# Kernel tuning notes

Measured on AMD Instinct MI355X. Metric: run time of the kernel, lower is better.

The kernel has to match this reference:

```python
import jax, jax.numpy as jnp
import numpy as np


def setup_inputs() -> dict:
    key = jax.random.key(0)
    ks = jax.random.split(key, 10)
    B, S, H, I, V = 64, 2048, 512, 512, 50257
    scale = 0.05
    return {
        "last_output": jax.random.randint(ks[0], (B,), 0, V),
        "last_hidden": jax.random.normal(ks[1], (1, B, H), jnp.float32),
        "encoder_outputs": jax.random.normal(ks[2], (S, B, H), jnp.float32),
        "embedding": jax.random.normal(ks[3], (V, I), jnp.float32) * scale,
        "W_ih": jax.random.normal(ks[4], (3 * H, I + H), jnp.float32) * scale,
        "b_ih": jax.random.normal(ks[5], (3 * H,), jnp.float32) * scale,
        "W_hh": jax.random.normal(ks[6], (3 * H, H), jnp.float32) * scale,
        "b_hh": jax.random.normal(ks[7], (3 * H,), jnp.float32) * scale,
        "W_out": jax.random.normal(ks[8], (V, 2 * H), jnp.float32) * scale,
        "b_out": jax.random.normal(ks[9], (V,), jnp.float32) * scale,
    }


def _gru_step(x, h, W_ih, b_ih, W_hh, b_hh):
    # torch nn.GRU parametrization, single layer, single timestep.
    H = h.shape[-1]
    gi = x @ W_ih.T + b_ih  # [B, 3H]
    gh = h @ W_hh.T + b_hh  # [B, 3H]
    i_r, i_z, i_n = gi[:, :H], gi[:, H:2 * H], gi[:, 2 * H:]
    h_r, h_z, h_n = gh[:, :H], gh[:, H:2 * H], gh[:, 2 * H:]
    r = jax.nn.sigmoid(i_r + h_r)
    z = jax.nn.sigmoid(i_z + h_z)
    n = jnp.tanh(i_n + r * h_n)
    return (1.0 - z) * n + z * h


def reference(last_output, last_hidden, encoder_outputs, embedding,
              W_ih, b_ih, W_hh, b_hh, W_out, b_out):
    # Embedding lookup: [B, I]
    embedded = embedding[last_output]
    h_top = last_hidden[-1]  # [B, H]
    # Luong 'dot' attention: score(b, s) = h_b . enc[s, b]
    scores = jnp.einsum('bh,sbh->bs', h_top, encoder_outputs)  # [B, S]
    attn = jax.nn.softmax(scores, axis=-1)                      # [B, S]
    # context = attn @ enc (per batch): [B, H]
    context = jnp.einsum('bs,sbh->bh', attn, encoder_outputs)
    # GRU single step on cat(embedded, context)
    rnn_in = jnp.concatenate([embedded, context], axis=-1)      # [B, I+H]
    h_new = _gru_step(rnn_in, h_top, W_ih, b_ih, W_hh, b_hh)    # [B, H]
    # Output projection on cat(rnn_out, context) -> log_softmax over vocab
    feat = jnp.concatenate([h_new, context], axis=-1)           # [B, 2H]
    logits = feat @ W_out.T + b_out                             # [B, V]
    logp = jax.nn.log_softmax(logits, axis=-1)
    hidden = h_new[None]  # [1, B, H]
    return logp, hidden
```

## Files before the change

kernel.cpp:

```cpp
#include <hip/hip_runtime.h>
#include <hip/hip_bf16.h>
#include <math.h>

#define BB 64
#define SS 2048
#define HH 512
#define VV 50257
#define KD 1024
#define NSPLIT 32
#define NTILE 786

typedef float f32x4 __attribute__((ext_vector_type(4)));
typedef __bf16 bf16x8 __attribute__((ext_vector_type(8)));

__device__ __forceinline__ float dot4(float4 a, float4 b) {
  return a.x*b.x + a.y*b.y + a.z*b.z + a.w*b.w;
}

__device__ __forceinline__ bf16x8 cvt8(float4 a, float4 b) {
  bf16x8 r;
  r[0]=(__bf16)a.x; r[1]=(__bf16)a.y; r[2]=(__bf16)a.z; r[3]=(__bf16)a.w;
  r[4]=(__bf16)b.x; r[5]=(__bf16)b.y; r[6]=(__bf16)b.z; r[7]=(__bf16)b.w;
  return r;
}

__device__ __forceinline__ size_t fragAddr(int b, int k) {
  return (size_t)(k >> 5)*2048 + (size_t)(b >> 4)*512
       + (size_t)((k >> 3) & 3)*128 + (size_t)(b & 15)*8 + (size_t)(k & 7);
}

__global__ __launch_bounds__(256) void attn_partial(
    const float* __restrict__ hprev, const float* __restrict__ enc,
    float* __restrict__ pm, float* __restrict__ pl, float* __restrict__ pacc)
{
  const int b = blockIdx.x >> 5;
  const int split = blockIdx.x & 31;
  const int t = threadIdx.x;
  const int w = t >> 6, lane = t & 63;

  const float* hb = hprev + b*HH + lane*8;
  const float4 h0 = *(const float4*)hb;
  const float4 h1 = *(const float4*)(hb + 4);
  const int s0 = split*64 + w*16;

  float m = -INFINITY, lsum = 0.f;
  float acc[8];
#pragma unroll
  for (int j = 0; j < 8; ++j) acc[j] = 0.f;

#pragma unroll 1
  for (int half = 0; half < 2; ++half) {
    float4 ea[8], eb[8];
#pragma unroll
    for (int i = 0; i < 8; ++i) {
      const float* ep = enc + ((size_t)(s0 + half*8 + i)*BB + b)*HH + lane*8;
      ea[i] = *(const float4*)ep; eb[i] = *(const float4*)(ep + 4);
    }
    float dd[8];
#pragma unroll
    for (int i = 0; i < 8; ++i) dd[i] = dot4(h0, ea[i]) + dot4(h1, eb[i]);
#pragma unroll
    for (int off = 32; off >= 1; off >>= 1) {
#pragma unroll
      for (int i = 0; i < 8; ++i) dd[i] += __shfl_xor(dd[i], off, 64);
    }
    float hm = dd[0];
#pragma unroll
    for (int i = 1; i < 8; ++i) hm = fmaxf(hm, dd[i]);
    const float mn = fmaxf(m, hm);
    const float sc = __expf(m - mn);
    float p[8], psum = 0.f;
#pragma unroll
    for (int i = 0; i < 8; ++i) { p[i] = __expf(dd[i] - mn); psum += p[i]; }
    lsum = lsum*sc + psum;
#pragma unroll
    for (int j = 0; j < 8; ++j) acc[j] *= sc;
#pragma unroll
    for (int i = 0; i < 8; ++i) {
      acc[0] += p[i]*ea[i].x; acc[1] += p[i]*ea[i].y;
      acc[2] += p[i]*ea[i].z; acc[3] += p[i]*ea[i].w;
      acc[4] += p[i]*eb[i].x; acc[5] += p[i]*eb[i].y;
      acc[6] += p[i]*eb[i].z; acc[7] += p[i]*eb[i].w;
    }
    m = mn;
  }

  __shared__ float sm4[4], sl4[4];
  __shared__ float sacc[4][HH];
  if (lane == 0) { sm4[w] = m; sl4[w] = lsum; }
  __syncthreads();
  const float M = fmaxf(fmaxf(sm4[0], sm4[1]), fmaxf(sm4[2], sm4[3]));
  const float ew = __expf(m - M);
#pragma unroll
  for (int j = 0; j < 8; ++j) sacc[w][lane*8 + j] = acc[j]*ew;
  __syncthreads();

  const int rec = blockIdx.x;
  for (int hh = t; hh < HH; hh += 256)
    pacc[(size_t)rec*HH + hh] = sacc[0][hh]+sacc[1][hh]+sacc[2][hh]+sacc[3][hh];
  if (t == 0) {
    float L = sl4[0]*__expf(sm4[0]-M) + sl4[1]*__expf(sm4[1]-M)
            + sl4[2]*__expf(sm4[2]-M) + sl4[3]*__expf(sm4[3]-M);
    pm[rec] = M; pl[rec] = L;
  }
}

__global__ __launch_bounds__(256) void attn_reduce(
    const float* __restrict__ pm, const float* __restrict__ pl,
    const float* __restrict__ pacc, __hip_bfloat16* __restrict__ featA)
{
  const int b = blockIdx.x, t = threadIdx.x;
  __shared__ float smm[NSPLIT], sll[NSPLIT], sco[NSPLIT];
  if (t < NSPLIT) { smm[t] = pm[b*NSPLIT + t]; sll[t] = pl[b*NSPLIT + t]; }
  __syncthreads();
  float M = -INFINITY;
  for (int q = 0; q < NSPLIT; ++q) M = fmaxf(M, smm[q]);
  float L = 0.f;
  for (int q = 0; q < NSPLIT; ++q) L += sll[q]*__expf(smm[q]-M);
  const float inv = 1.f/L;
  if (t < NSPLIT) sco[t] = __expf(smm[t]-M)*inv;
  __syncthreads();
  const int hh0 = 2*t;
  float s0 = 0.f, s1 = 0.f;
  for (int q = 0; q < NSPLIT; ++q) {
    const float* pq = pacc + ((size_t)b*NSPLIT + q)*HH;
    s0 += pq[hh0]   * sco[q];
    s1 += pq[hh0+1] * sco[q];
  }
  const size_t a = fragAddr(b, HH + hh0);
  featA[a]   = (__hip_bfloat16)s0;
  featA[a+1] = (__hip_bfloat16)s1;
}

__global__ __launch_bounds__(256) void gru_gemm(
    const int* __restrict__ last_out, const float* __restrict__ emb,
    const float* __restrict__ hprev, const __hip_bfloat16* __restrict__ featA,
    const float* __restrict__ W_ih, const float* __restrict__ W_hh,
    float* __restrict__ gates)
{
  const int u = blockIdx.x;
  const int gt = u / 12;
  const int rem = u % 12;
  const int seg = rem >> 2, ks = rem & 3;
  const int w = threadIdx.x >> 6, lane = threadIdx.x & 63;
  const int col = lane & 15, kg = lane >> 4;
  const int g = gt*64 + w*16 + col;

  const float* wrow = (seg == 2) ? (W_hh + (size_t)g*HH)
                                 : (W_ih + (size_t)g*KD + seg*HH);
  int lo_r[4];
#pragma unroll
  for (int mt = 0; mt < 4; ++mt) lo_r[mt] = last_out[mt*16 + col];

  f32x4 acc[4];
#pragma unroll
  for (int mt = 0; mt < 4; ++mt) acc[mt] = (f32x4){0.f,0.f,0.f,0.f};

  const int kbeg = ks*128, kend = kbeg + 128;
  for (int k0 = kbeg; k0 < kend; k0 += 32) {
    const float* wp = wrow + k0 + kg*8;
    const bf16x8 bf = cvt8(*(const float4*)wp, *(const float4*)(wp+4));
#pragma unroll
    for (int mt = 0; mt < 4; ++mt) {
      const int bb = mt*16 + col;
      bf16x8 af;
      if (seg == 0) {
        const float* ap = emb + (size_t)lo_r[mt]*HH + k0 + kg*8;
        af = cvt8(*(const float4*)ap, *(const float4*)(ap+4));
      } else if (seg == 1) {
        af = *(const bf16x8*)(featA + fragAddr(bb, HH + k0 + kg*8));
      } else {
        const float* ap = hprev + (size_t)bb*HH + k0 + kg*8;
        af = cvt8(*(const float4*)ap, *(const float4*)(ap+4));
      }
      acc[mt] = __builtin_amdgcn_mfma_f32_16x16x32_bf16(af, bf, acc[mt], 0, 0, 0);
    }
  }

  float* gp = gates + (size_t)rem*BB*1536;
#pragma unroll
  for (int mt = 0; mt < 4; ++mt)
#pragma unroll
    for (int reg = 0; reg < 4; ++reg) {
      const int brow = mt*16 + kg*4 + reg;
      gp[(size_t)brow*1536 + g] = acc[mt][reg];
    }
}

__global__ __launch_bounds__(512) void gru_pointwise(
    const float* __restrict__ gates, const float* __restrict__ hprev,
    const float* __restrict__ b_ih, const float* __restrict__ b_hh,
    float* __restrict__ hid_out, __hip_bfloat16* __restrict__ featA)
{
  const int b = blockIdx.x, j = threadIdx.x;

  float i_r = 0.f, i_z = 0.f, i_n = 0.f;
#pragma unroll
  for (int p = 0; p < 8; ++p) {
    const float* gp = gates + ((size_t)p*BB + b)*1536;
    i_r += gp[j]; i_z += gp[HH + j]; i_n += gp[2*HH + j];
  }
  float h_r = 0.f, h_z = 0.f, h_n = 0.f;
#pragma unroll
  for (int p = 8; p < 12; ++p) {
    const float* gp = gates + ((size_t)p*BB + b)*1536;
    h_r += gp[j]; h_z += gp[HH + j]; h_n += gp[2*HH + j];
  }

  const float r = 1.f/(1.f + __expf(-(i_r + h_r + b_ih[j] + b_hh[j])));
  const float z = 1.f/(1.f + __expf(-(i_z + h_z + b_ih[HH+j] + b_hh[HH+j])));
  const float n = tanhf(i_n + b_ih[2*HH+j] + r*(h_n + b_hh[2*HH+j]));
  const float hp = hprev[b*HH + j];
  const float hn = (1.f - z)*n + z*hp;
  hid_out[b*HH + j] = hn;
  featA[fragAddr(b, j)] = (__hip_bfloat16)hn;
}

__global__ __launch_bounds__(256) void logits_gemm(
    const __hip_bfloat16* __restrict__ featA, const float* __restrict__ W_out,
    const float* __restrict__ b_out, float* __restrict__ out,
    float* __restrict__ pmE, float* __restrict__ plE)
{
  __shared__ float vals[64*65];
  __shared__ float pMq[4*64], pLq[4*64];
  const int tile = blockIdx.x;
  const int t = threadIdx.x;
  const int w = t >> 6, lane = t & 63;
  const int col = lane & 15, kg = lane >> 4;
  const int v = tile*64 + w*16 + col;
  const int vc = (v < VV) ? v : (VV - 1);

  const float* wp = W_out + (size_t)vc*KD + kg*8;
  const __hip_bfloat16* fp = featA + lane*8;

  f32x4 acc[4];
#pragma unroll
  for (int mt = 0; mt < 4; ++mt) acc[mt] = (f32x4){0.f,0.f,0.f,0.f};

  float4 WA[3], WB[3];
  bf16x8 AF[3][4];

#pragma unroll
  for (int s = 0; s < 2; ++s) {
    WA[s] = *(const float4*)(wp + s*32);
    WB[s] = *(const float4*)(wp + s*32 + 4);
    const __hip_bfloat16* f = fp + s*2048;
    AF[s][0] = *(const bf16x8*)(f);
    AF[s][1] = *(const bf16x8*)(f + 512);
    AF[s][2] = *(const bf16x8*)(f + 1024);
    AF[s][3] = *(const bf16x8*)(f + 1536);
  }

#pragma unroll
  for (int kc = 0; kc < 32; ++kc) {
    if (kc + 2 < 32) {
      const int s = (kc + 2) % 3;
      WA[s] = *(const float4*)(wp + (kc+2)*32);
      WB[s] = *(const float4*)(wp + (kc+2)*32 + 4);
      const __hip_bfloat16* f = fp + (kc+2)*2048;
      AF[s][0] = *(const bf16x8*)(f);
      AF[s][1] = *(const bf16x8*)(f + 512);
      AF[s][2] = *(const bf16x8*)(f + 1024);
      AF[s][3] = *(const bf16x8*)(f + 1536);
    }
    const int c = kc % 3;
    const bf16x8 bf = cvt8(WA[c], WB[c]);
    acc[0] = __builtin_amdgcn_mfma_f32_16x16x32_bf16(AF[c][0], bf, acc[0], 0, 0, 0);
    acc[1] = __builtin_amdgcn_mfma_f32_16x16x32_bf16(AF[c][1], bf, acc[1], 0, 0, 0);
    acc[2] = __builtin_amdgcn_mfma_f32_16x16x32_bf16(AF[c][2], bf, acc[2], 0, 0, 0);
    acc[3] = __builtin_amdgcn_mfma_f32_16x16x32_bf16(AF[c][3], bf, acc[3], 0, 0, 0);
  }

  const float bo = (v < VV) ? b_out[v] : 0.f;
#pragma unroll
  for (int mt = 0; mt < 4; ++mt)
#pragma unroll
    for (int reg = 0; reg < 4; ++reg) {
      const float val = acc[mt][reg] + bo;
      const int brow = mt*16 + kg*4 + reg;
      if (v < VV) out[(size_t)brow*VV + v] = val;
      vals[brow*65 + w*16 + col] = (v < VV) ? val : -INFINITY;
    }
  __syncthreads();

  {
    const int row = t & 63, q = t >> 6;
    const float* vr = vals + row*65 + q*16;
    float M = -INFINITY;
#pragma unroll
    for (int i = 0; i < 16; ++i) M = fmaxf(M, vr[i]);
    float L = 0.f;
    if (M > -INFINITY) {
#pragma unroll
      for (int i = 0; i < 16; ++i) L += __expf(vr[i] - M);
    }
    pMq[q*64 + row] = M; pLq[q*64 + row] = L;
  }
  __syncthreads();
  if (t < 64) {
    float M = pMq[t], L = pLq[t];
#pragma unroll
    for (int q = 1; q < 4; ++q) {
      const float mq = pMq[q*64 + t], lq = pLq[q*64 + t];
      if (mq > -INFINITY) {
        const float mn = fmaxf(M, mq);
        L = L*__expf(M - mn) + lq*__expf(mq - mn);
        M = mn;
      }
    }
    pmE[t*1024 + tile] = M; plE[t*1024 + tile] = L;
  }
}

__global__ __launch_bounds__(256) void lsm_sub(
    float* __restrict__ out, const float* __restrict__ pmE,
    const float* __restrict__ plE)
{
  const int t = threadIdx.x;
  const int wv = t >> 6, lane = t & 63;
  const size_t off = (size_t)blockIdx.x * 1024;
  const size_t total = (size_t)BB*VV;
  __shared__ float cs[2];
  __shared__ int rowA_s;

  if (wv < 2) {
    size_t pos = (wv == 0) ? off : (off + 1023 < total ? off + 1023 : total - 1);
    const int row = (int)(pos / VV);
    float M = -INFINITY, L = 0.f;
    for (int q = lane; q < NTILE; q += 64) {
      const float mq = pmE[row*1024 + q], lq = plE[row*1024 + q];
      const float mn = fmaxf(M, mq);
      L = L*__expf(M - mn) + lq*__expf(mq - mn);
      M = mn;
    }
#pragma unroll
    for (int o = 32; o >= 1; o >>= 1) {
      const float m2 = __shfl_xor(M, o, 64), l2 = __shfl_xor(L, o, 64);
      const float mn = fmaxf(M, m2);
      L = L*__expf(M - mn) + l2*__expf(m2 - mn);
      M = mn;
    }
    if (lane == 0) {
      cs[wv] = M + logf(L);
      if (wv == 0) rowA_s = row;
    }
  }
  __syncthreads();

  const size_t i = off + (size_t)t*4;
  if (i >= total) return;
  const size_t rs = (size_t)(rowA_s + 1)*VV;
  float4 v = *(float4*)(out + i);
  v.x -= (i     >= rs) ? cs[1] : cs[0];
  v.y -= (i + 1 >= rs) ? cs[1] : cs[0];
  v.z -= (i + 2 >= rs) ? cs[1] : cs[0];
  v.w -= (i + 3 >= rs) ? cs[1] : cs[0];
  *(float4*)(out + i) = v;
}

extern "C" void kernel_launch(void* const* d_in, const int* in_sizes, int n_in,
                              void* d_out, int out_size, void* d_ws, size_t ws_size,
                              hipStream_t stream)
{
  const int*   last_output = (const int*)d_in[0];
  const float* last_hidden = (const float*)d_in[1];
  const float* enc         = (const float*)d_in[2];
  const float* emb         = (const float*)d_in[3];
  const float* W_ih        = (const float*)d_in[4];
  const float* b_ih        = (const float*)d_in[5];
  const float* W_hh        = (const float*)d_in[6];
  const float* b_hh        = (const float*)d_in[7];
  const float* W_out       = (const float*)d_in[8];
  const float* b_out       = (const float*)d_in[9];
  float* out = (float*)d_out;

  __hip_bfloat16* featA = (__hip_bfloat16*)d_ws;
  float* gates = (float*)((char*)d_ws + 131072);
  float* pm   = gates + (size_t)12*BB*1536;
  float* pl   = pm + BB*NSPLIT;
  float* pmE  = pl + BB*NSPLIT;
  float* plE  = pmE + BB*1024;
  float* pacc = out;
  float* hid_out = out + (size_t)BB*VV;

  attn_partial <<<dim3(BB*NSPLIT), dim3(256), 0, stream>>>(last_hidden, enc, pm, pl, pacc);
  attn_reduce  <<<dim3(BB),        dim3(256), 0, stream>>>(pm, pl, pacc, featA);
  gru_gemm     <<<dim3(24*12),     dim3(256), 0, stream>>>(last_output, emb, last_hidden,
                                                           featA, W_ih, W_hh, gates);
  gru_pointwise<<<dim3(BB),        dim3(512), 0, stream>>>(gates, last_hidden, b_ih, b_hh,
                                                           hid_out, featA);
  logits_gemm  <<<dim3(NTILE),     dim3(256), 0, stream>>>(featA, W_out, b_out, out, pmE, plE);
  lsm_sub      <<<dim3((int)(((size_t)BB*VV + 1023)/1024)), dim3(256), 0, stream>>>(out, pmE, plE);
}
```

Baseline: 163.6 us.

## Stage W_out tiles into LDS via async global_load_lds with double buffering

The logits GEMM now loads W_out tiles with global_load_lds straight into a swizzled, double-buffered shared-memory buffer instead of per-thread register prefetch. Each wave then reads its fragments from LDS with an XOR swizzle meant to avoid bank conflicts, and the feature fragments are read directly from global memory each step. The goal is more coalesced loads of the large W_out matrix and overlap of loading with MFMA work. In exchange it adds a barrier per k-chunk and a larger shared-memory footprint, which may lower occupancy.

```diff
diff --git a/kernel.cpp b/kernel.cpp
--- a/kernel.cpp
+++ b/kernel.cpp
@@ -12,6 +12,8 @@
 
 typedef float f32x4 __attribute__((ext_vector_type(4)));
 typedef __bf16 bf16x8 __attribute__((ext_vector_type(8)));
+typedef __attribute__((address_space(3))) void lds_void;
+typedef __attribute__((address_space(1))) const void glb_void;
 
 __device__ __forceinline__ float dot4(float4 a, float4 b) {
   return a.x*b.x + a.y*b.y + a.z*b.z + a.w*b.w;
@@ -221,56 +223,62 @@
     const float* __restrict__ b_out, float* __restrict__ out,
     float* __restrict__ pmE, float* __restrict__ plE)
 {
-  __shared__ float vals[64*65];
+  __shared__ float smem[8192];
   __shared__ float pMq[4*64], pLq[4*64];
   const int tile = blockIdx.x;
   const int t = threadIdx.x;
   const int w = t >> 6, lane = t & 63;
   const int col = lane & 15, kg = lane >> 4;
-  const int v = tile*64 + w*16 + col;
-  const int vc = (v < VV) ? v : (VV - 1);
-
-  const float* wp = W_out + (size_t)vc*KD + kg*8;
+  const int vbase = tile*64;
+  const int v = vbase + w*16 + col;
+
   const __hip_bfloat16* fp = featA + lane*8;
+  const int rowL = w*16 + col;
+  const int sXor = (rowL & 7) << 2;
+
+  auto stage = [&](int buf, int kc) {
+#pragma unroll
+    for (int i = 0; i < 4; ++i) {
+      const int sigma = (w*4 + i)*64 + lane;
+      const int row = sigma >> 4;
+      const int t16 = sigma & 15;
+      const int kdl = (t16*4) ^ ((row & 7) << 2);
+      int grow = vbase + row; if (grow > VV-1) grow = VV-1;
+      const float* src = W_out + (size_t)grow*KD + kc*64 + kdl;
+      __builtin_amdgcn_global_load_lds((glb_void*)src,
+          (lds_void*)(smem + buf*4096 + (w*4 + i)*256), 16, 0, 0);
+    }
+  };
 
   f32x4 acc[4];
 #pragma unroll
   for (int mt = 0; mt < 4; ++mt) acc[mt] = (f32x4){0.f,0.f,0.f,0.f};
 
-  float4 WA[3], WB[3];
-  bf16x8 AF[3][4];
-
-#pragma unroll
-  for (int s = 0; s < 2; ++s) {
-    WA[s] = *(const float4*)(wp + s*32);
-    WB[s] = *(const float4*)(wp + s*32 + 4);
-    const __hip_bfloat16* f = fp + s*2048;
-    AF[s][0] = *(const bf16x8*)(f);
-    AF[s][1] = *(const bf16x8*)(f + 512);
-    AF[s][2] = *(const bf16x8*)(f + 1024);
-    AF[s][3] = *(const bf16x8*)(f + 1536);
-  }
-
-#pragma unroll
-  for (int kc = 0; kc < 32; ++kc) {
-    if (kc + 2 < 32) {
-      const int s = (kc + 2) % 3;
-      WA[s] = *(const float4*)(wp + (kc+2)*32);
-      WB[s] = *(const float4*)(wp + (kc+2)*32 + 4);
-      const __hip_bfloat16* f = fp + (kc+2)*2048;
-      AF[s][0] = *(const bf16x8*)(f);
-      AF[s][1] = *(const bf16x8*)(f + 512);
-      AF[s][2] = *(const bf16x8*)(f + 1024);
-      AF[s][3] = *(const bf16x8*)(f + 1536);
-    }
-    const int c = kc % 3;
-    const bf16x8 bf = cvt8(WA[c], WB[c]);
-    acc[0] = __builtin_amdgcn_mfma_f32_16x16x32_bf16(AF[c][0], bf, acc[0], 0, 0, 0);
-    acc[1] = __builtin_amdgcn_mfma_f32_16x16x32_bf16(AF[c][1], bf, acc[1], 0, 0, 0);
-    acc[2] = __builtin_amdgcn_mfma_f32_16x16x32_bf16(AF[c][2], bf, acc[2], 0, 0, 0);
-    acc[3] = __builtin_amdgcn_mfma_f32_16x16x32_bf16(AF[c][3], bf, acc[3], 0, 0, 0);
-  }
-
+  int buf = 0;
+  stage(0, 0);
+  __syncthreads();
+
+#pragma unroll 1
+  for (int kc = 0; kc < 16; ++kc) {
+    if (kc + 1 < 16) stage(buf ^ 1, kc + 1);
+    const float* wt = smem + buf*4096;
+#pragma unroll
+    for (int h = 0; h < 2; ++h) {
+      const int kin = h*32 + kg*8;
+      const float4 wa = *(const float4*)(wt + rowL*64 + (kin ^ sXor));
+      const float4 wb = *(const float4*)(wt + rowL*64 + ((kin + 4) ^ sXor));
+      const bf16x8 bf = cvt8(wa, wb);
+      const __hip_bfloat16* f = fp + (size_t)(kc*2 + h)*2048;
+      acc[0] = __builtin_amdgcn_mfma_f32_16x16x32_bf16(*(const bf16x8*)(f),        bf, acc[0], 0, 0, 0);
+      acc[1] = __builtin_amdgcn_mfma_f32_16x16x32_bf16(*(const bf16x8*)(f + 512),  bf, acc[1], 0, 0, 0);
+      acc[2] = __builtin_amdgcn_mfma_f32_16x16x32_bf16(*(const bf16x8*)(f + 1024), bf, acc[2], 0, 0, 0);
+      acc[3] = __builtin_amdgcn_mfma_f32_16x16x32_bf16(*(const bf16x8*)(f + 1536), bf, acc[3], 0, 0, 0);
+    }
+    __syncthreads();
+    buf ^= 1;
+  }
+
+  float* vals = smem;
   const float bo = (v < VV) ? b_out[v] : 0.f;
 #pragma unroll
   for (int mt = 0; mt < 4; ++mt)
```

Measured after the change: 157.7 us. 3.6% less time.
